# Kernel optimization log

Measured on AMD Instinct MI355X. Metric: run time of the kernel, lower is better.

Reference implementation:

```python
import jax, jax.numpy as jnp
import numpy as np

B, T, IN, OUT = 131072, 8, 128, 128


def setup_inputs() -> dict:
    key = jax.random.key(0)
    k1, k2, k3, k4 = jax.random.split(key, 4)
    x = jax.random.normal(k1, (B, IN), dtype=jnp.float32)
    types = jax.random.randint(k2, (B,), 0, T, dtype=jnp.int64)
    # xavier_uniform over (out, in) fan dims
    limit = float(np.sqrt(6.0 / (IN + OUT)))
    W = jax.random.uniform(k3, (T, OUT, IN), dtype=jnp.float32, minval=-limit, maxval=limit)
    b = jnp.zeros((T, OUT), dtype=jnp.float32)
    return {"x": x, "types": types, "W": W, "b": b}


def reference(x, types, W, b):
    # y[i] = W[types[i]] @ x[i] + b[types[i]]
    # Compute all-type projections [B, T, OUT], then select per-token type.
    # This avoids materializing the huge [B, OUT, IN] gathered weight tensor.
    y_all = jnp.einsum("bi,toi->bto", x, W)           # [B, T, OUT]
    y = jnp.take_along_axis(y_all, types[:, None, None].astype(jnp.int32), axis=1)[:, 0, :]
    return y + b[types]
```

## Files before the change

kernel.cpp:

```cpp
#include <hip/hip_runtime.h>
#include <hip/hip_bf16.h>


typedef __attribute__((ext_vector_type(8))) short bf16x8;
typedef __attribute__((ext_vector_type(4))) float f32x4;
typedef __attribute__((ext_vector_type(4))) float float4v;

static constexpr int kBT = 128;
static constexpr int kT  = 8;
static constexpr int kD  = 128;

__device__ __forceinline__ short f2bf(float f) {
  union { __hip_bfloat16 h; short u; } cv;
  cv.h = __float2bfloat16(f);
  return cv.u;
}

__global__ __launch_bounds__(256) void wconv_kernel(const float* __restrict__ W,
                                                    short* __restrict__ Wb) {
  const int i = (blockIdx.x * 256 + threadIdx.x) * 8;
  float4v a = *(const float4v*)(W + i);
  float4v b = *(const float4v*)(W + i + 4);
  bf16x8 r;
  r[0] = f2bf(a[0]); r[1] = f2bf(a[1]); r[2] = f2bf(a[2]); r[3] = f2bf(a[3]);
  r[4] = f2bf(b[0]); r[5] = f2bf(b[1]); r[6] = f2bf(b[2]); r[7] = f2bf(b[3]);
  *(bf16x8*)(Wb + i) = r;
}

__global__ __launch_bounds__(256, 4) void typed_linear_kernel(
    const float* __restrict__ x, const int* __restrict__ types,
    const short* __restrict__ Wb, const float* __restrict__ bias,
    float* __restrict__ y) {
  __shared__ int s_cnt[kT];
  __shared__ unsigned char s_list[kT][kBT];

  const int tid = threadIdx.x;
  if (tid < kT) s_cnt[tid] = 0;
  __syncthreads();
  const int tok0 = blockIdx.x * kBT;
  if (tid < kBT) {
    const int t = types[tok0 + tid];
    const int pos = atomicAdd(&s_cnt[t], 1);
    s_list[t][pos] = (unsigned char)tid;
  }
  __syncthreads();

  const int w    = tid >> 6;
  const int lane = tid & 63;
  const int lr   = lane & 15;
  const int lg   = lane >> 4;

  for (int t = 0; t < kT; ++t) {
    const int cnt = s_cnt[t];
    if (cnt == 0) continue;

    bf16x8 bfr[2][4];
    const short* wrow = Wb + ((t * kD + w * 32 + lr) * kD);
#pragma unroll
    for (int c = 0; c < 2; ++c)
#pragma unroll
      for (int s = 0; s < 4; ++s)
        bfr[c][s] = *(const bf16x8*)(wrow + c * 16 * kD + s * 32 + lg * 8);

    const float bias0 = bias[t * kD + w * 32 + lr];
    const float bias1 = bias[t * kD + w * 32 + 16 + lr];

    for (int m0 = 0; m0 < cnt; m0 += 16) {
      int ia = m0 + lr;
      ia = ia < cnt ? ia : cnt - 1;
      const float* xr = x + (size_t)(tok0 + s_list[t][ia]) * kD;
      bf16x8 afr[4];
#pragma unroll
      for (int s = 0; s < 4; ++s) {
        float4v u0 = *(const float4v*)(xr + s * 32 + lg * 8);
        float4v u1 = *(const float4v*)(xr + s * 32 + lg * 8 + 4);
        bf16x8 a;
        a[0] = f2bf(u0[0]); a[1] = f2bf(u0[1]); a[2] = f2bf(u0[2]); a[3] = f2bf(u0[3]);
        a[4] = f2bf(u1[0]); a[5] = f2bf(u1[1]); a[6] = f2bf(u1[2]); a[7] = f2bf(u1[3]);
        afr[s] = a;
      }

      f32x4 acc0 = {0.f, 0.f, 0.f, 0.f};
      f32x4 acc1 = {0.f, 0.f, 0.f, 0.f};
#pragma unroll
      for (int s = 0; s < 4; ++s) {
        acc0 = __builtin_amdgcn_mfma_f32_16x16x32_bf16(afr[s], bfr[0][s], acc0, 0, 0, 0);
        acc1 = __builtin_amdgcn_mfma_f32_16x16x32_bf16(afr[s], bfr[1][s], acc1, 0, 0, 0);
      }

#pragma unroll
      for (int r = 0; r < 4; ++r) {
        const int rl = lg * 4 + r;
        if (m0 + rl < cnt) {
          float* yp = y + (size_t)(tok0 + s_list[t][m0 + rl]) * kD + w * 32 + lr;
          yp[0]  = acc0[r] + bias0;
          yp[16] = acc1[r] + bias1;
        }
      }
    }
  }
}

extern "C" void kernel_launch(void* const* d_in, const int* in_sizes, int n_in,
                              void* d_out, int out_size, void* d_ws, size_t ws_size,
                              hipStream_t stream) {
  const float* x     = (const float*)d_in[0];
  const int*   types = (const int*)d_in[1];
  const float* W     = (const float*)d_in[2];
  const float* bias  = (const float*)d_in[3];
  float*       y     = (float*)d_out;
  short*       Wb    = (short*)d_ws;

  const int n_tok = in_sizes[0] / kD;

  wconv_kernel<<<(kT * kD * kD) / (256 * 8), 256, 0, stream>>>(W, Wb);
  typed_linear_kernel<<<n_tok / kBT, 256, 0, stream>>>(x, types, Wb, bias, y);
}
```

Before: 166.7 us.

## Stage x tiles into LDS via async global_load_lds with double buffering

Each block now handles 256 tokens as four 64-token tiles. Tile i+1 is loaded from x into a double-buffered, XOR-swizzled LDS region with global_load_lds while tile i is computed. The A fragments are then read from LDS instead of being gathered with scattered global loads per type. This costs 64KB of LDS per block, fewer blocks, and occupancy hints lowered to 2 per SIMD. Per-tile type lists add more weight-fragment reloads per block.

Result: slower. 171.1 us (+2.6%).

```diff
diff --git a/kernel.cpp b/kernel.cpp
--- a/kernel.cpp
+++ b/kernel.cpp
@@ -6,9 +6,12 @@
 typedef __attribute__((ext_vector_type(4))) float f32x4;
 typedef __attribute__((ext_vector_type(4))) float float4v;
 
-static constexpr int kBT = 128;
-static constexpr int kT  = 8;
-static constexpr int kD  = 128;
+static constexpr int kT       = 8;
+static constexpr int kD       = 128;
+static constexpr int kTileTok = 64;
+static constexpr int kTiles   = 4;
+static constexpr int kBlkTok  = kTileTok * kTiles;
+static constexpr int kThreads = 256;
 
 __device__ __forceinline__ short f2bf(float f) {
   union { __hip_bfloat16 h; short u; } cv;
@@ -27,74 +30,104 @@
   *(bf16x8*)(Wb + i) = r;
 }
 
-__global__ __launch_bounds__(256, 4) void typed_linear_kernel(
+__global__ __launch_bounds__(kThreads, 2) void typed_linear_kernel(
     const float* __restrict__ x, const int* __restrict__ types,
     const short* __restrict__ Wb, const float* __restrict__ bias,
     float* __restrict__ y) {
-  __shared__ int s_cnt[kT];
-  __shared__ unsigned char s_list[kT][kBT];
+  __shared__ float xb[2][kTileTok * kD];
+  __shared__ int s_cnt[kTiles][kT];
+  __shared__ unsigned char s_list[kTiles][kT][kTileTok];
 
-  const int tid = threadIdx.x;
-  if (tid < kT) s_cnt[tid] = 0;
+  const int tid   = threadIdx.x;
+  const long tok0 = (long)blockIdx.x * kBlkTok;
+
+  if (tid < kTiles * kT) ((int*)s_cnt)[tid] = 0;
   __syncthreads();
-  const int tok0 = blockIdx.x * kBT;
-  if (tid < kBT) {
-    const int t = types[tok0 + tid];
-    const int pos = atomicAdd(&s_cnt[t], 1);
-    s_list[t][pos] = (unsigned char)tid;
+  {
+    const int t    = types[tok0 + tid];
+    const int tile = tid >> 6;
+    const int pos  = atomicAdd(&s_cnt[tile][t], 1);
+    s_list[tile][t][pos] = (unsigned char)(tid & 63);
   }
-  __syncthreads();
 
   const int w    = tid >> 6;
   const int lane = tid & 63;
   const int lr   = lane & 15;
   const int lg   = lane >> 4;
 
-  for (int t = 0; t < kT; ++t) {
-    const int cnt = s_cnt[t];
-    if (cnt == 0) continue;
+  auto dma_tile = [&](int buf, int tile) {
+    const float* xt = x + (tok0 + (long)tile * kTileTok) * kD;
+#pragma unroll
+    for (int j = 0; j < 8; ++j) {
+      const int rp = w * 8 + j;
+      const int r  = rp * 2 + (lane >> 5);
+      const int p  = lane & 31;
+      const float* src = xt + r * kD + ((p ^ (r & 7)) << 2);
+      float* dst = &xb[buf][rp * 2 * kD];
+      __builtin_amdgcn_global_load_lds(
+          (const __attribute__((address_space(1))) void*)src,
+          (__attribute__((address_space(3))) void*)dst, 16, 0, 0);
+    }
+  };
 
-    bf16x8 bfr[2][4];
-    const short* wrow = Wb + ((t * kD + w * 32 + lr) * kD);
+  dma_tile(0, 0);
+
+  for (int i = 0; i < kTiles; ++i) {
+    __syncthreads();
+    if (i + 1 < kTiles) dma_tile((i + 1) & 1, i + 1);
+
+    const float* xt   = xb[i & 1];
+    const long ytile0 = tok0 + (long)i * kTileTok;
+
+    for (int t = 0; t < kT; ++t) {
+      const int cnt = s_cnt[i][t];
+      if (cnt == 0) continue;
+
+      bf16x8 bfr[2][4];
+      const short* wrow = Wb + ((t * kD + w * 32 + lr) * kD);
 #pragma unroll
-    for (int c = 0; c < 2; ++c)
+      for (int c = 0; c < 2; ++c)
 #pragma unroll
-      for (int s = 0; s < 4; ++s)
-        bfr[c][s] = *(const bf16x8*)(wrow + c * 16 * kD + s * 32 + lg * 8);
+        for (int s = 0; s < 4; ++s)
+          bfr[c][s] = *(const bf16x8*)(wrow + c * 16 * kD + s * 32 + lg * 8);
 
-    const float bias0 = bias[t * kD + w * 32 + lr];
-    const float bias1 = bias[t * kD + w * 32 + 16 + lr];
+      const float bias0 = bias[t * kD + w * 32 + lr];
+      const float bias1 = bias[t * kD + w * 32 + 16 + lr];
 
-    for (int m0 = 0; m0 < cnt; m0 += 16) {
-      int ia = m0 + lr;
-      ia = ia < cnt ? ia : cnt - 1;
-      const float* xr = x + (size_t)(tok0 + s_list[t][ia]) * kD;
-      bf16x8 afr[4];
+      for (int m0 = 0; m0 < cnt; m0 += 16) {
+        int ia = m0 + lr;
+        ia = ia < cnt ? ia : cnt - 1;
+        const int row = s_list[i][t][ia];
+        const int m7  = row & 7;
+
+        bf16x8 afr[4];
 #pragma unroll
-      for (int s = 0; s < 4; ++s) {
-        float4v u0 = *(const float4v*)(xr + s * 32 + lg * 8);
-        float4v u1 = *(const float4v*)(xr + s * 32 + lg * 8 + 4);
-        bf16x8 a;
-        a[0] = f2bf(u0[0]); a[1] = f2bf(u0[1]); a[2] = f2bf(u0[2]); a[3] = f2bf(u0[3]);
-        a[4] = f2bf(u1[0]); a[5] = f2bf(u1[1]); a[6] = f2bf(u1[2]); a[7] = f2bf(u1[3]);
-        afr[s] = a;
-      }
+        for (int s = 0; s < 4; ++s) {
+          const int g = s * 8 + lg * 2;
+          const float4v lo = *(const float4v*)(xt + row * kD + ((g ^ m7) << 2));
+          const float4v hi = *(const float4v*)(xt + row * kD + (((g + 1) ^ m7) << 2));
+          bf16x8 a;
+          a[0] = f2bf(lo[0]); a[1] = f2bf(lo[1]); a[2] = f2bf(lo[2]); a[3] = f2bf(lo[3]);
+          a[4] = f2bf(hi[0]); a[5] = f2bf(hi[1]); a[6] = f2bf(hi[2]); a[7] = f2bf(hi[3]);
+          afr[s] = a;
+        }
 
-      f32x4 acc0 = {0.f, 0.f, 0.f, 0.f};
-      f32x4 acc1 = {0.f, 0.f, 0.f, 0.f};
+        f32x4 acc0 = {0.f, 0.f, 0.f, 0.f};
+        f32x4 acc1 = {0.f, 0.f, 0.f, 0.f};
 #pragma unroll
-      for (int s = 0; s < 4; ++s) {
-        acc0 = __builtin_amdgcn_mfma_f32_16x16x32_bf16(afr[s], bfr[0][s], acc0, 0, 0, 0);
-        acc1 = __builtin_amdgcn_mfma_f32_16x16x32_bf16(afr[s], bfr[1][s], acc1, 0, 0, 0);
-      }
+        for (int s = 0; s < 4; ++s) {
+          acc0 = __builtin_amdgcn_mfma_f32_16x16x32_bf16(afr[s], bfr[0][s], acc0, 0, 0, 0);
+          acc1 = __builtin_amdgcn_mfma_f32_16x16x32_bf16(afr[s], bfr[1][s], acc1, 0, 0, 0);
+        }
 
 #pragma unroll
-      for (int r = 0; r < 4; ++r) {
-        const int rl = lg * 4 + r;
-        if (m0 + rl < cnt) {
-          float* yp = y + (size_t)(tok0 + s_list[t][m0 + rl]) * kD + w * 32 + lr;
-          yp[0]  = acc0[r] + bias0;
-          yp[16] = acc1[r] + bias1;
+        for (int r = 0; r < 4; ++r) {
+          const int rl = lg * 4 + r;
+          if (m0 + rl < cnt) {
+            float* yp = y + (ytile0 + s_list[i][t][m0 + rl]) * kD + w * 32 + lr;
+            yp[0]  = acc0[r] + bias0;
+            yp[16] = acc1[r] + bias1;
+          }
         }
       }
     }
@@ -114,5 +147,5 @@
   const int n_tok = in_sizes[0] / kD;
 
   wconv_kernel<<<(kT * kD * kD) / (256 * 8), 256, 0, stream>>>(W, Wb);
-  typed_linear_kernel<<<n_tok / kBT, 256, 0, stream>>>(x, types, Wb, bias, y);
+  typed_linear_kernel<<<n_tok / kBlkTok, kThreads, 0, stream>>>(x, types, Wb, bias, y);
 }
```
